# Performance work log

Hardware: AMD Instinct MI355X
Metric: run time of the kernel (lower is better)

## Reference

```python
import jax, jax.numpy as jnp
import numpy as np

IN_FEATURES = 4096
OUT_FEATURES = 4096
NUM_GROUPS = 32
HARDTANH_MIN = -2.0
HARDTANH_MAX = 2.0
EPS = 1e-6


def setup_inputs() -> dict:
    key = jax.random.key(0)
    k1, k2 = jax.random.split(key)
    x = jax.random.normal(k1, (8192, IN_FEATURES), dtype=jnp.float32)
    W = jax.random.normal(k2, (OUT_FEATURES, IN_FEATURES), dtype=jnp.float32)
    b = jnp.zeros((OUT_FEATURES,), dtype=jnp.float32)
    return {"x": x, "W": W, "b": b}


def reference(x, W, b):
    B = x.shape[0]
    group_size = OUT_FEATURES // NUM_GROUPS
    # GEMM: y[b, n] = sum_k x[b, k] * W[n, k]
    y = jnp.einsum("bk,nk->bn", x, W)
    # GroupNorm over each group of channels per row (no affine scale)
    yg = y.reshape(B, NUM_GROUPS, group_size)
    mean = jnp.mean(yg, axis=2, keepdims=True)
    var = jnp.mean((yg - mean) ** 2, axis=2, keepdims=True)
    norm = (yg - mean) / jnp.sqrt(var + EPS)
    norm = norm.reshape(B, OUT_FEATURES) + b[None, :]
    # kernel clamps to [-2, 2], then outer clamp to [hardtanh_min, hardtanh_max]
    out = jnp.clip(norm, -2.0, 2.0)
    out = jnp.clip(out, HARDTANH_MIN, HARDTANH_MAX)
    return out
```

## Files before the change

### kernel.cpp

```cpp
#include <hip/hip_runtime.h>
#include <hip/hip_bf16.h>
#include <stdint.h>

#define M_DIM 8192
#define N_DIM 4096
#define K_DIM 4096
#define BM 256
#define BN 256
#define BK 32
#define NT (K_DIM / BK)

typedef __attribute__((ext_vector_type(8))) short short8;
typedef __attribute__((ext_vector_type(4))) float f32x4;
typedef unsigned short ushort_t;

__device__ __forceinline__ ushort_t f2bf(float f) {
    uint32_t u = __float_as_uint(f);
    uint32_t r = (u + 0x7FFFu + ((u >> 16) & 1u)) >> 16;
    return (ushort_t)r;
}

__global__ void cvt_f32_bf16(const float4* __restrict__ in, ushort* __restrict__ out4, int n4) {
    int i = blockIdx.x * blockDim.x + threadIdx.x;
    if (i < n4) {
        float4 v = in[i];
        ushort_t a = f2bf(v.x), b = f2bf(v.y), c = f2bf(v.z), d = f2bf(v.w);
        uint32_t lo = (uint32_t)a | ((uint32_t)b << 16);
        uint32_t hi = (uint32_t)c | ((uint32_t)d << 16);
        uint2* o = reinterpret_cast<uint2*>(out4);
        o[i] = make_uint2(lo, hi);
    }
}

__device__ __forceinline__ void gload_lds16(const ushort_t* g, void* l) {
    __builtin_amdgcn_global_load_lds(
        (const __attribute__((address_space(1))) unsigned int*)g,
        (__attribute__((address_space(3))) unsigned int*)l,
        16, 0, 0);
}

__global__ __launch_bounds__(512, 2)
void gemm_gn_kernel(const ushort_t* __restrict__ xb,
                    const ushort_t* __restrict__ wb,
                    const float*   __restrict__ bias,
                    float*         __restrict__ out)
{
    __shared__ char pool[3 * 32768];

    const int tid = threadIdx.x;
    const int w   = tid >> 6;
    const int l   = tid & 63;
    const int wr  = w >> 2;
    const int wc  = w & 3;
    const int l15 = l & 15;
    const int l4  = l >> 4;

    const int TN = N_DIM / BN;
    int bid = blockIdx.x;
    bid = (bid & 7) * ((M_DIM / BM) * TN / 8) + (bid >> 3);
    const int brow = (bid / TN) * BM;
    const int bcol = (bid % TN) * BN;

    const int srow  = tid >> 2;
    const int sslot = (tid & 3) ^ (srow & 3);
    const ushort_t* gA0 = xb + (size_t)(brow + srow)       * K_DIM + sslot * 8;
    const ushort_t* gA1 = xb + (size_t)(brow + 128 + srow) * K_DIM + sslot * 8;
    const ushort_t* gB0 = wb + (size_t)(bcol + srow)       * K_DIM + sslot * 8;
    const ushort_t* gB1 = wb + (size_t)(bcol + 128 + srow) * K_DIM + sslot * 8;

    f32x4 acc[8][4];
#pragma unroll
    for (int i = 0; i < 8; ++i)
#pragma unroll
        for (int j = 0; j < 4; ++j) acc[i][j] = (f32x4){0.f, 0.f, 0.f, 0.f};

    auto STAGE = [&](char* buf, int t) {
        const int k0 = t * BK;
        char* ldsA = buf + w * 1024;
        gload_lds16(gA0 + k0, ldsA);
        gload_lds16(gA1 + k0, ldsA + 8192);
        char* ldsB = buf + 16384 + w * 1024;
        gload_lds16(gB0 + k0, ldsB);
        gload_lds16(gB1 + k0, ldsB + 8192);
    };

    const int sw = ((l4 ^ (l15 & 3)) << 4);
    const int arow0 = wr * 128 + l15;
    const int brow0 = wc * 64 + l15;

    auto COMPUTE = [&](char* buf) {
        const char* A = buf;
        const char* B = buf + 16384;
        short8 af[8], bf[4];
#pragma unroll
        for (int mi = 0; mi < 8; ++mi)
            af[mi] = *(const short8*)(A + (arow0 + mi * 16) * 64 + sw);
#pragma unroll
        for (int ni = 0; ni < 4; ++ni)
            bf[ni] = *(const short8*)(B + (brow0 + ni * 16) * 64 + sw);
        __builtin_amdgcn_s_setprio(1);
#pragma unroll
        for (int mi = 0; mi < 8; ++mi)
#pragma unroll
            for (int ni = 0; ni < 4; ++ni)
                acc[mi][ni] = __builtin_amdgcn_mfma_f32_16x16x32_bf16(
                    af[mi], bf[ni], acc[mi][ni], 0, 0, 0);
        __builtin_amdgcn_s_setprio(0);
    };

    char* b0 = pool;
    char* b1 = pool + 32768;
    char* b2 = pool + 65536;
    STAGE(b0, 0);
    STAGE(b1, 1);
    STAGE(b2, 2);
    char* cur = b0; char* nxt = b1; char* fut = b2;

    for (int t = 0; t < NT; ++t) {
        if (t < NT - 2)       { asm volatile("s_waitcnt vmcnt(8)" ::: "memory"); }
        else if (t == NT - 2) { asm volatile("s_waitcnt vmcnt(4)" ::: "memory"); }
        else                  { asm volatile("s_waitcnt vmcnt(0)" ::: "memory"); }
        asm volatile("s_barrier" ::: "memory");

        COMPUTE(cur);

        asm volatile("s_waitcnt lgkmcnt(0)" ::: "memory");
        asm volatile("s_barrier" ::: "memory");
        if (t + 3 < NT) STAGE(cur, t + 3);
        char* tmp = cur; cur = nxt; nxt = fut; fut = tmp;
    }

    float s[8][4], s2[8][4];
#pragma unroll
    for (int mi = 0; mi < 8; ++mi)
#pragma unroll
        for (int r = 0; r < 4; ++r) {
            float a = 0.f, b = 0.f;
#pragma unroll
            for (int ni = 0; ni < 4; ++ni) {
                float v = acc[mi][ni][r];
                a += v;
                b += v * v;
            }
#pragma unroll
            for (int m = 1; m < 16; m <<= 1) {
                a += __shfl_xor(a, m);
                b += __shfl_xor(b, m);
            }
            s[mi][r] = a;
            s2[mi][r] = b;
        }

    float* redS  = (float*)pool;
    float* redS2 = (float*)(pool + 4096);
    if (l15 == 0) {
#pragma unroll
        for (int mi = 0; mi < 8; ++mi)
#pragma unroll
            for (int r = 0; r < 4; ++r) {
                int R = wr * 128 + mi * 16 + l4 * 4 + r;
                redS [R * 4 + wc] = s[mi][r];
                redS2[R * 4 + wc] = s2[mi][r];
            }
    }
    __syncthreads();

    float bv[4];
#pragma unroll
    for (int ni = 0; ni < 4; ++ni)
        bv[ni] = bias[bcol + wc * 64 + ni * 16 + l15];

    const int g2 = (wc >> 1) * 2;
    const float inv_gs = 1.0f / 128.0f;
#pragma unroll
    for (int mi = 0; mi < 8; ++mi)
#pragma unroll
        for (int r = 0; r < 4; ++r) {
            int R = wr * 128 + mi * 16 + l4 * 4 + r;
            float S  = redS [R * 4 + g2] + redS [R * 4 + g2 + 1];
            float S2 = redS2[R * 4 + g2] + redS2[R * 4 + g2 + 1];
            float mean = S * inv_gs;
            float var  = S2 * inv_gs - mean * mean;
            float inv  = rsqrtf(var + 1e-6f);
            size_t rowbase = (size_t)(brow + R) * N_DIM + bcol + wc * 64 + l15;
#pragma unroll
            for (int ni = 0; ni < 4; ++ni) {
                float v = (acc[mi][ni][r] - mean) * inv + bv[ni];
                v = fminf(fmaxf(v, -2.0f), 2.0f);
                out[rowbase + ni * 16] = v;
            }
        }
}

extern "C" void kernel_launch(void* const* d_in, const int* in_sizes, int n_in,
                              void* d_out, int out_size, void* d_ws, size_t ws_size,
                              hipStream_t stream) {
    const float* x = (const float*)d_in[0];
    const float* W = (const float*)d_in[1];
    const float* b = (const float*)d_in[2];
    float* out = (float*)d_out;

    ushort_t* xb = (ushort_t*)d_ws;
    ushort_t* wb = xb + (size_t)M_DIM * K_DIM;

    int n4x = M_DIM * K_DIM / 4;
    cvt_f32_bf16<<<(n4x + 255) / 256, 256, 0, stream>>>(
        (const float4*)x, xb, n4x);
    int n4w = N_DIM * K_DIM / 4;
    cvt_f32_bf16<<<(n4w + 255) / 256, 256, 0, stream>>>(
        (const float4*)W, wb, n4w);

    int grid = (M_DIM / BM) * (N_DIM / BN);
    gemm_gn_kernel<<<grid, 512, 0, stream>>>(xb, wb, b, out);
}
```

Measured before the change: 367.1 us.

## Restructure GEMM main loop into four-phase double-buffered BK=64 schedule

Raises the K tile from 32 to 64 and replaces the triple-buffered single-phase loop with a double-buffered loop split into four quadrant phases. Each phase loads part of the A/B fragments from LDS, issues a quarter of the next tile's global-to-LDS loads, and runs a quarter of the MFMAs. The aim is finer interleaving of memory traffic with compute and half as many outer iterations. It uses 128KB of LDS, which may reduce occupancy below the 2 blocks per CU requested in the launch bounds, and adds more barriers per iteration.

Result: faster. 326.0 us (-11.2%).

```diff
diff --git a/kernel.cpp b/kernel.cpp
--- a/kernel.cpp
+++ b/kernel.cpp
@@ -7,12 +7,15 @@
 #define K_DIM 4096
 #define BM 256
 #define BN 256
-#define BK 32
-#define NT (K_DIM / BK)
+#define BK 64
+#define NTILES (K_DIM / BK)
 
 typedef __attribute__((ext_vector_type(8))) short short8;
 typedef __attribute__((ext_vector_type(4))) float f32x4;
 typedef unsigned short ushort_t;
+
+#define SBAR()      asm volatile("s_barrier" ::: "memory")
+#define WAIT_LGKM0() asm volatile("s_waitcnt lgkmcnt(0)" ::: "memory")
 
 __device__ __forceinline__ ushort_t f2bf(float f) {
     uint32_t u = __float_as_uint(f);
@@ -45,7 +48,7 @@
                     const float*   __restrict__ bias,
                     float*         __restrict__ out)
 {
-    __shared__ char pool[3 * 32768];
+    __shared__ char pool[131072];
 
     const int tid = threadIdx.x;
     const int w   = tid >> 6;
@@ -61,12 +64,19 @@
     const int brow = (bid / TN) * BM;
     const int bcol = (bid % TN) * BN;
 
-    const int srow  = tid >> 2;
-    const int sslot = (tid & 3) ^ (srow & 3);
-    const ushort_t* gA0 = xb + (size_t)(brow + srow)       * K_DIM + sslot * 8;
-    const ushort_t* gA1 = xb + (size_t)(brow + 128 + srow) * K_DIM + sslot * 8;
-    const ushort_t* gB0 = wb + (size_t)(bcol + srow)       * K_DIM + sslot * 8;
-    const ushort_t* gB1 = wb + (size_t)(bcol + 128 + srow) * K_DIM + sslot * 8;
+    const int srow8 = tid >> 3;
+    const int sslot = (tid & 7) ^ (srow8 & 7);
+    const ushort_t* gA = xb + (size_t)(brow + srow8) * K_DIM + sslot * 8;
+    const ushort_t* gB = wb + (size_t)(bcol + srow8) * K_DIM + sslot * 8;
+    const size_t ROW64 = (size_t)64 * K_DIM;
+    const int wave1024 = w * 1024;
+
+    auto STAGE = [&](int buf, int isB, int h, int kt) {
+        const ushort_t* src = (isB ? gB : gA) + (size_t)h * 128 * K_DIM + (size_t)kt * 64;
+        char* dst = pool + buf * 65536 + isB * 32768 + h * 16384 + wave1024;
+        gload_lds16(src, dst);
+        gload_lds16(src + ROW64, dst + 8192);
+    };
 
     f32x4 acc[8][4];
 #pragma unroll
@@ -74,61 +84,101 @@
 #pragma unroll
         for (int j = 0; j < 4; ++j) acc[i][j] = (f32x4){0.f, 0.f, 0.f, 0.f};
 
-    auto STAGE = [&](char* buf, int t) {
-        const int k0 = t * BK;
-        char* ldsA = buf + w * 1024;
-        gload_lds16(gA0 + k0, ldsA);
-        gload_lds16(gA1 + k0, ldsA + 8192);
-        char* ldsB = buf + 16384 + w * 1024;
-        gload_lds16(gB0 + k0, ldsB);
-        gload_lds16(gB1 + k0, ldsB + 8192);
-    };
-
-    const int sw = ((l4 ^ (l15 & 3)) << 4);
-    const int arow0 = wr * 128 + l15;
-    const int brow0 = wc * 64 + l15;
-
-    auto COMPUTE = [&](char* buf) {
-        const char* A = buf;
-        const char* B = buf + 16384;
-        short8 af[8], bf[4];
-#pragma unroll
-        for (int mi = 0; mi < 8; ++mi)
-            af[mi] = *(const short8*)(A + (arow0 + mi * 16) * 64 + sw);
-#pragma unroll
-        for (int ni = 0; ni < 4; ++ni)
-            bf[ni] = *(const short8*)(B + (brow0 + ni * 16) * 64 + sw);
-        __builtin_amdgcn_s_setprio(1);
-#pragma unroll
-        for (int mi = 0; mi < 8; ++mi)
-#pragma unroll
-            for (int ni = 0; ni < 4; ++ni)
-                acc[mi][ni] = __builtin_amdgcn_mfma_f32_16x16x32_bf16(
-                    af[mi], bf[ni], acc[mi][ni], 0, 0, 0);
-        __builtin_amdgcn_s_setprio(0);
-    };
-
-    char* b0 = pool;
-    char* b1 = pool + 32768;
-    char* b2 = pool + 65536;
-    STAGE(b0, 0);
-    STAGE(b1, 1);
-    STAGE(b2, 2);
-    char* cur = b0; char* nxt = b1; char* fut = b2;
-
-    for (int t = 0; t < NT; ++t) {
-        if (t < NT - 2)       { asm volatile("s_waitcnt vmcnt(8)" ::: "memory"); }
-        else if (t == NT - 2) { asm volatile("s_waitcnt vmcnt(4)" ::: "memory"); }
-        else                  { asm volatile("s_waitcnt vmcnt(0)" ::: "memory"); }
-        asm volatile("s_barrier" ::: "memory");
-
-        COMPUTE(cur);
-
-        asm volatile("s_waitcnt lgkmcnt(0)" ::: "memory");
-        asm volatile("s_barrier" ::: "memory");
-        if (t + 3 < NT) STAGE(cur, t + 3);
-        char* tmp = cur; cur = nxt; nxt = fut; fut = tmp;
+    const int swz = (l15 & 7) << 4;
+    const int x0  = (l4 * 16) ^ swz;
+    const int x1  = (64 + l4 * 16) ^ swz;
+    const int abase = (wr * 128 + l15) * 128;
+    const int bbase = (wc * 64  + l15) * 128;
+
+    STAGE(0, 1, 0, 0); STAGE(0, 1, 1, 0);
+    STAGE(0, 0, 0, 0); STAGE(0, 0, 1, 0);
+    STAGE(1, 1, 0, 1); STAGE(1, 1, 1, 1);
+    asm volatile("s_waitcnt vmcnt(4)" ::: "memory");
+    SBAR();
+
+    short8 af[8], bf[8];
+
+    for (int T = 0; T < NTILES; ++T) {
+        const char* Ab = pool + (T & 1) * 65536;
+        const char* Bb = Ab + 32768;
+
+#pragma unroll
+        for (int m = 0; m < 4; ++m) {
+            af[m * 2]     = *(const short8*)(Ab + abase + m * 2048 + x0);
+            af[m * 2 + 1] = *(const short8*)(Ab + abase + m * 2048 + x1);
+        }
+#pragma unroll
+        for (int n = 0; n < 2; ++n) {
+            bf[n * 2]     = *(const short8*)(Bb + bbase + n * 2048 + x0);
+            bf[n * 2 + 1] = *(const short8*)(Bb + bbase + n * 2048 + x1);
+        }
+        if (T + 1 < NTILES) STAGE((T + 1) & 1, 0, 0, T + 1);
+        asm volatile("s_waitcnt lgkmcnt(8)" ::: "memory");
+        SBAR(); WAIT_LGKM0();
+        __builtin_amdgcn_s_setprio(1);
+#pragma unroll
+        for (int m = 0; m < 4; ++m)
+#pragma unroll
+            for (int n = 0; n < 2; ++n) {
+                acc[m][n] = __builtin_amdgcn_mfma_f32_16x16x32_bf16(af[m*2],   bf[n*2],   acc[m][n], 0, 0, 0);
+                acc[m][n] = __builtin_amdgcn_mfma_f32_16x16x32_bf16(af[m*2+1], bf[n*2+1], acc[m][n], 0, 0, 0);
+            }
+        __builtin_amdgcn_s_setprio(0);
+        SBAR();
+
+#pragma unroll
+        for (int n = 2; n < 4; ++n) {
+            bf[n * 2]     = *(const short8*)(Bb + bbase + n * 2048 + x0);
+            bf[n * 2 + 1] = *(const short8*)(Bb + bbase + n * 2048 + x1);
+        }
+        if (T + 1 < NTILES) STAGE((T + 1) & 1, 0, 1, T + 1);
+        SBAR(); WAIT_LGKM0();
+        __builtin_amdgcn_s_setprio(1);
+#pragma unroll
+        for (int m = 0; m < 4; ++m)
+#pragma unroll
+            for (int n = 2; n < 4; ++n) {
+                acc[m][n] = __builtin_amdgcn_mfma_f32_16x16x32_bf16(af[m*2],   bf[n*2],   acc[m][n], 0, 0, 0);
+                acc[m][n] = __builtin_amdgcn_mfma_f32_16x16x32_bf16(af[m*2+1], bf[n*2+1], acc[m][n], 0, 0, 0);
+            }
+        __builtin_amdgcn_s_setprio(0);
+        SBAR();
+
+#pragma unroll
+        for (int m = 0; m < 4; ++m) {
+            af[m * 2]     = *(const short8*)(Ab + abase + (m + 4) * 2048 + x0);
+            af[m * 2 + 1] = *(const short8*)(Ab + abase + (m + 4) * 2048 + x1);
+        }
+        if (T + 2 < NTILES) STAGE(T & 1, 1, 0, T + 2);
+        SBAR(); WAIT_LGKM0();
+        __builtin_amdgcn_s_setprio(1);
+#pragma unroll
+        for (int m = 0; m < 4; ++m)
+#pragma unroll
+            for (int n = 0; n < 2; ++n) {
+                acc[4+m][n] = __builtin_amdgcn_mfma_f32_16x16x32_bf16(af[m*2],   bf[n*2],   acc[4+m][n], 0, 0, 0);
+                acc[4+m][n] = __builtin_amdgcn_mfma_f32_16x16x32_bf16(af[m*2+1], bf[n*2+1], acc[4+m][n], 0, 0, 0);
+            }
+        __builtin_amdgcn_s_setprio(0);
+        SBAR();
+
+        if (T + 2 < NTILES) STAGE(T & 1, 1, 1, T + 2);
+        if (T < NTILES - 2) { asm volatile("s_waitcnt vmcnt(4)" ::: "memory"); }
+        else                { asm volatile("s_waitcnt vmcnt(0)" ::: "memory"); }
+        SBAR();
+        __builtin_amdgcn_s_setprio(1);
+#pragma unroll
+        for (int m = 0; m < 4; ++m)
+#pragma unroll
+            for (int n = 2; n < 4; ++n) {
+                acc[4+m][n] = __builtin_amdgcn_mfma_f32_16x16x32_bf16(af[m*2],   bf[n*2],   acc[4+m][n], 0, 0, 0);
+                acc[4+m][n] = __builtin_amdgcn_mfma_f32_16x16x32_bf16(af[m*2+1], bf[n*2+1], acc[4+m][n], 0, 0, 0);
+            }
+        __builtin_amdgcn_s_setprio(0);
+        SBAR();
     }
+
+    __syncthreads();
 
     float s[8][4], s2[8][4];
 #pragma unroll
```

## Restructure GEMM into 4-wave 256x256 tiles with BK=64 ping-pong quadrant pipeline

Applied to the files above, without the earlier changes.

Moves from 8 waves with 128x64 per-wave tiles and a triple-buffered BK=32 loop to 4 waves, each owning a 128x128 tile, with BK=64 and a double-buffered schedule. Each K step is split into four MFMA quadrants interleaved with LDS fragment reads and global-to-LDS staging, to hide load latency and cut the number of barriers per unit of work. Because each wave now covers a full 128-column group, the GroupNorm reduction no longer needs an LDS cross-wave exchange. The risks are higher register pressure from 64 accumulators at occupancy 1, and correctness of the hand-tuned waitcnt and barrier ordering.

Result: faster. 311.6 us (-15.1%).

```diff
diff --git a/kernel.cpp b/kernel.cpp
--- a/kernel.cpp
+++ b/kernel.cpp
@@ -7,12 +7,17 @@
 #define K_DIM 4096
 #define BM 256
 #define BN 256
-#define BK 32
-#define NT (K_DIM / BK)
+#define BK 64
+#define NT 64
 
 typedef __attribute__((ext_vector_type(8))) short short8;
 typedef __attribute__((ext_vector_type(4))) float f32x4;
 typedef unsigned short ushort_t;
+
+#define SBAR()  asm volatile("s_barrier" ::: "memory")
+#define LGKM(n) asm volatile("s_waitcnt lgkmcnt(" #n ")" ::: "memory")
+#define VM(n)   asm volatile("s_waitcnt vmcnt(" #n ")" ::: "memory")
+#define SCHEDB() __builtin_amdgcn_sched_barrier(0)
 
 __device__ __forceinline__ ushort_t f2bf(float f) {
     uint32_t u = __float_as_uint(f);
@@ -39,105 +44,156 @@
         16, 0, 0);
 }
 
-__global__ __launch_bounds__(512, 2)
+__global__ __launch_bounds__(256, 1)
 void gemm_gn_kernel(const ushort_t* __restrict__ xb,
                     const ushort_t* __restrict__ wb,
                     const float*   __restrict__ bias,
                     float*         __restrict__ out)
 {
-    __shared__ char pool[3 * 32768];
+    __shared__ char pool[131072];
 
     const int tid = threadIdx.x;
     const int w   = tid >> 6;
     const int l   = tid & 63;
-    const int wr  = w >> 2;
-    const int wc  = w & 3;
+    const int wr  = w >> 1;
+    const int wc  = w & 1;
     const int l15 = l & 15;
     const int l4  = l >> 4;
 
     const int TN = N_DIM / BN;
     int bid = blockIdx.x;
-    bid = (bid & 7) * ((M_DIM / BM) * TN / 8) + (bid >> 3);
+    bid = (bid & 7) * 64 + (bid >> 3);
     const int brow = (bid / TN) * BM;
     const int bcol = (bid % TN) * BN;
 
-    const int srow  = tid >> 2;
-    const int sslot = (tid & 3) ^ (srow & 3);
-    const ushort_t* gA0 = xb + (size_t)(brow + srow)       * K_DIM + sslot * 8;
-    const ushort_t* gA1 = xb + (size_t)(brow + 128 + srow) * K_DIM + sslot * 8;
-    const ushort_t* gB0 = wb + (size_t)(bcol + srow)       * K_DIM + sslot * 8;
-    const ushort_t* gB1 = wb + (size_t)(bcol + 128 + srow) * K_DIM + sslot * 8;
-
-    f32x4 acc[8][4];
+    const int srow  = tid >> 3;
+    const int sslot = (tid & 7) ^ (srow & 7);
+    const ushort_t* gA = xb + (size_t)(brow + srow) * K_DIM + sslot * 8;
+    const ushort_t* gB = wb + (size_t)(bcol + srow) * K_DIM + sslot * 8;
+    const int wbase = w * 1024;
+
+    auto STAGE_A = [&](int buf, int half, int kt) {
+        const ushort_t* s = gA + (size_t)half * 128 * K_DIM + (size_t)kt * 64;
+        char* d = pool + buf * 65536 + half * 16384 + wbase;
+        gload_lds16(s,                      d);
+        gload_lds16(s + (size_t)32 * K_DIM, d + 4096);
+        gload_lds16(s + (size_t)64 * K_DIM, d + 8192);
+        gload_lds16(s + (size_t)96 * K_DIM, d + 12288);
+    };
+    auto STAGE_B = [&](int buf, int half, int kt) {
+        const ushort_t* s = gB + (size_t)half * 128 * K_DIM + (size_t)kt * 64;
+        char* d = pool + buf * 65536 + 32768 + half * 16384 + wbase;
+        gload_lds16(s,                      d);
+        gload_lds16(s + (size_t)32 * K_DIM, d + 4096);
+        gload_lds16(s + (size_t)64 * K_DIM, d + 8192);
+        gload_lds16(s + (size_t)96 * K_DIM, d + 12288);
+    };
+
+    const int swz = (l15 & 7) << 4;
+    const int x0  = (l4 * 16) ^ swz;
+    const int x1  = (64 + l4 * 16) ^ swz;
+    const int abase = (wr * 128 + l15) * 128;
+    const int bbase = (wc * 128 + l15) * 128;
+
+    short8 afL[8], afH[8], bfL[8], bfH[8];
+
+    auto RD_A = [&](short8* dst, const char* Ab, int mi0) {
+#pragma unroll
+        for (int m = 0; m < 4; ++m) {
+            dst[m * 2]     = *(const short8*)(Ab + abase + (mi0 + m) * 2048 + x0);
+            dst[m * 2 + 1] = *(const short8*)(Ab + abase + (mi0 + m) * 2048 + x1);
+        }
+    };
+    auto RD_B = [&](short8* dst, const char* Bb, int ni0) {
+#pragma unroll
+        for (int n = 0; n < 4; ++n) {
+            dst[n * 2]     = *(const short8*)(Bb + bbase + (ni0 + n) * 2048 + x0);
+            dst[n * 2 + 1] = *(const short8*)(Bb + bbase + (ni0 + n) * 2048 + x1);
+        }
+    };
+
+    f32x4 acc[8][8];
 #pragma unroll
     for (int i = 0; i < 8; ++i)
 #pragma unroll
-        for (int j = 0; j < 4; ++j) acc[i][j] = (f32x4){0.f, 0.f, 0.f, 0.f};
-
-    auto STAGE = [&](char* buf, int t) {
-        const int k0 = t * BK;
-        char* ldsA = buf + w * 1024;
-        gload_lds16(gA0 + k0, ldsA);
-        gload_lds16(gA1 + k0, ldsA + 8192);
-        char* ldsB = buf + 16384 + w * 1024;
-        gload_lds16(gB0 + k0, ldsB);
-        gload_lds16(gB1 + k0, ldsB + 8192);
-    };
-
-    const int sw = ((l4 ^ (l15 & 3)) << 4);
-    const int arow0 = wr * 128 + l15;
-    const int brow0 = wc * 64 + l15;
-
-    auto COMPUTE = [&](char* buf) {
-        const char* A = buf;
-        const char* B = buf + 16384;
-        short8 af[8], bf[4];
-#pragma unroll
-        for (int mi = 0; mi < 8; ++mi)
-            af[mi] = *(const short8*)(A + (arow0 + mi * 16) * 64 + sw);
-#pragma unroll
-        for (int ni = 0; ni < 4; ++ni)
-            bf[ni] = *(const short8*)(B + (brow0 + ni * 16) * 64 + sw);
-        __builtin_amdgcn_s_setprio(1);
-#pragma unroll
-        for (int mi = 0; mi < 8; ++mi)
-#pragma unroll
-            for (int ni = 0; ni < 4; ++ni)
-                acc[mi][ni] = __builtin_amdgcn_mfma_f32_16x16x32_bf16(
-                    af[mi], bf[ni], acc[mi][ni], 0, 0, 0);
-        __builtin_amdgcn_s_setprio(0);
-    };
-
-    char* b0 = pool;
-    char* b1 = pool + 32768;
-    char* b2 = pool + 65536;
-    STAGE(b0, 0);
-    STAGE(b1, 1);
-    STAGE(b2, 2);
-    char* cur = b0; char* nxt = b1; char* fut = b2;
-
-    for (int t = 0; t < NT; ++t) {
-        if (t < NT - 2)       { asm volatile("s_waitcnt vmcnt(8)" ::: "memory"); }
-        else if (t == NT - 2) { asm volatile("s_waitcnt vmcnt(4)" ::: "memory"); }
-        else                  { asm volatile("s_waitcnt vmcnt(0)" ::: "memory"); }
-        asm volatile("s_barrier" ::: "memory");
-
-        COMPUTE(cur);
-
-        asm volatile("s_waitcnt lgkmcnt(0)" ::: "memory");
-        asm volatile("s_barrier" ::: "memory");
-        if (t + 3 < NT) STAGE(cur, t + 3);
-        char* tmp = cur; cur = nxt; nxt = fut; fut = tmp;
+        for (int j = 0; j < 8; ++j) acc[i][j] = (f32x4){0.f, 0.f, 0.f, 0.f};
+
+    auto MM = [&](short8* A, short8* B, int m0, int n0) {
+#pragma unroll
+        for (int k = 0; k < 2; ++k)
+#pragma unroll
+            for (int m = 0; m < 4; ++m)
+#pragma unroll
+                for (int n = 0; n < 4; ++n)
+                    acc[m0 + m][n0 + n] = __builtin_amdgcn_mfma_f32_16x16x32_bf16(
+                        A[m * 2 + k], B[n * 2 + k], acc[m0 + m][n0 + n], 0, 0, 0);
+    };
+
+    STAGE_A(0, 0, 0); STAGE_A(0, 1, 0);
+    STAGE_B(0, 0, 0); STAGE_B(0, 1, 0);
+    STAGE_B(1, 0, 1); STAGE_B(1, 1, 1);
+    VM(8);
+    SBAR();
+    RD_B(bfL, pool + 32768, 0);
+    RD_A(afL, pool, 0);
+
+    for (int T = 0; T < NT; ++T) {
+        const int cb = T & 1;
+        const char* Ab = pool + cb * 65536;
+        const char* Bb = Ab + 32768;
+        const char* Abn = pool + (cb ^ 1) * 65536;
+        const char* Bbn = Abn + 32768;
+
+        SBAR();
+        RD_A(afH, Ab, 4);
+        if (T + 1 < NT) STAGE_A(cb ^ 1, 0, T + 1);
+        LGKM(8);
+        SCHEDB();
+        __builtin_amdgcn_s_setprio(1);
+        MM(afL, bfL, 0, 0);
+        __builtin_amdgcn_s_setprio(0);
+
+        SBAR();
+        RD_B(bfH, Bb, 4);
+        if (T + 1 < NT) STAGE_A(cb ^ 1, 1, T + 1);
+        LGKM(8);
+        SCHEDB();
+        __builtin_amdgcn_s_setprio(1);
+        MM(afH, bfL, 4, 0);
+        __builtin_amdgcn_s_setprio(0);
+
+        if (T + 2 < NT) STAGE_B(cb, 0, T + 2);
+        LGKM(0);
+        if (T < NT - 2) { VM(8); } else { VM(0); }
+        SBAR();
+        SCHEDB();
+        if (T + 1 < NT) RD_B(bfL, Bbn, 0);
+        __builtin_amdgcn_s_setprio(1);
+        MM(afH, bfH, 4, 4);
+        __builtin_amdgcn_s_setprio(0);
+
+        if (T + 2 < NT) STAGE_B(cb, 1, T + 2);
+        if (T < NT - 2) { VM(8); } else { VM(0); }
+        SBAR();
+        __builtin_amdgcn_s_setprio(1);
+        MM(afL, bfH, 0, 4);
+        __builtin_amdgcn_s_setprio(0);
+        if (T + 1 < NT) RD_A(afL, Abn, 0);
     }
 
-    float s[8][4], s2[8][4];
-#pragma unroll
-    for (int mi = 0; mi < 8; ++mi)
+    float bv[8];
+#pragma unroll
+    for (int ni = 0; ni < 8; ++ni)
+        bv[ni] = bias[bcol + wc * 128 + ni * 16 + l15];
+
+    const float inv_gs = 1.0f / 128.0f;
+#pragma unroll
+    for (int mi = 0; mi < 8; ++mi) {
 #pragma unroll
         for (int r = 0; r < 4; ++r) {
             float a = 0.f, b = 0.f;
 #pragma unroll
-            for (int ni = 0; ni < 4; ++ni) {
+            for (int ni = 0; ni < 8; ++ni) {
                 float v = acc[mi][ni][r];
                 a += v;
                 b += v * v;
@@ -147,49 +203,19 @@
                 a += __shfl_xor(a, m);
                 b += __shfl_xor(b, m);
             }
-            s[mi][r] = a;
-            s2[mi][r] = b;
-        }
-
-    float* redS  = (float*)pool;
-    float* redS2 = (float*)(pool + 4096);
-    if (l15 == 0) {
-#pragma unroll
-        for (int mi = 0; mi < 8; ++mi)
-#pragma unroll
-            for (int r = 0; r < 4; ++r) {
-                int R = wr * 128 + mi * 16 + l4 * 4 + r;
-                redS [R * 4 + wc] = s[mi][r];
-                redS2[R * 4 + wc] = s2[mi][r];
-            }
-    }
-    __syncthreads();
-
-    float bv[4];
-#pragma unroll
-    for (int ni = 0; ni < 4; ++ni)
-        bv[ni] = bias[bcol + wc * 64 + ni * 16 + l15];
-
-    const int g2 = (wc >> 1) * 2;
-    const float inv_gs = 1.0f / 128.0f;
-#pragma unroll
-    for (int mi = 0; mi < 8; ++mi)
-#pragma unroll
-        for (int r = 0; r < 4; ++r) {
+            float mean = a * inv_gs;
+            float var  = b * inv_gs - mean * mean;
+            float inv  = rsqrtf(var + 1e-6f);
             int R = wr * 128 + mi * 16 + l4 * 4 + r;
-            float S  = redS [R * 4 + g2] + redS [R * 4 + g2 + 1];
-            float S2 = redS2[R * 4 + g2] + redS2[R * 4 + g2 + 1];
-            float mean = S * inv_gs;
-            float var  = S2 * inv_gs - mean * mean;
-            float inv  = rsqrtf(var + 1e-6f);
-            size_t rowbase = (size_t)(brow + R) * N_DIM + bcol + wc * 64 + l15;
-#pragma unroll
-            for (int ni = 0; ni < 4; ++ni) {
+            size_t rowbase = (size_t)(brow + R) * N_DIM + bcol + wc * 128 + l15;
+#pragma unroll
+            for (int ni = 0; ni < 8; ++ni) {
                 float v = (acc[mi][ni][r] - mean) * inv + bv[ni];
                 v = fminf(fmaxf(v, -2.0f), 2.0f);
                 out[rowbase + ni * 16] = v;
             }
         }
+    }
 }
 
 extern "C" void kernel_launch(void* const* d_in, const int* in_sizes, int n_in,
@@ -211,5 +237,5 @@
         (const float4*)W, wb, n4w);
 
     int grid = (M_DIM / BM) * (N_DIM / BN);
-    gemm_gn_kernel<<<grid, 512, 0, stream>>>(xb, wb, b, out);
-}
+    gemm_gn_kernel<<<grid, 256, 0, stream>>>(xb, wb, b, out);
+}
```
